# Optimization experiments

Measured on AMD Instinct MI355X. Metric: run time of the kernel, lower is better.

The kernel has to match this reference:

```python
import jax, jax.numpy as jnp
import numpy as np
from jax import lax

NL, DM, DI, DS, DTR, NC = 4, 128, 256, 16, 8, 256  # layers, d_model, d_inner, d_state, dt_rank, classes
B, L = 24, 3072  # conv stride 3 -> T = 1024


def _ln(x, w, b, eps=1e-5):
    mu = x.mean(-1, keepdims=True)
    v = ((x - mu) ** 2).mean(-1, keepdims=True)
    return (x - mu) * lax.rsqrt(v + eps) * w + b


def _mixer(h, inp, cw, cb, xp, dtw, dtb, Alog, D):
    # h: (B,T,DM) -> Mamba selective-scan mixer output (B,T,DI) before out_proj
    xz = h @ inp.T                                   # (B,T,2*DI)
    x, z = jnp.split(xz, 2, axis=-1)
    # causal depthwise conv (torch pads d_conv-1=3 both sides then slices [:T] == left-pad 3)
    xc = lax.conv_general_dilated(x.transpose(0, 2, 1), cw, (1,), [(3, 0)],
                                  feature_group_count=DI,
                                  dimension_numbers=('NCH', 'OIH', 'NCH'))
    xc = jax.nn.silu((xc + cb[None, :, None]).transpose(0, 2, 1))   # (B,T,DI)
    dbl = xc @ xp.T                                  # (B,T,DTR+2*DS)
    dt = jax.nn.softplus(dbl[..., :DTR] @ dtw.T + dtb)              # (B,T,DI)
    Bm, Cm = dbl[..., DTR:DTR + DS], dbl[..., DTR + DS:]            # (B,T,DS) each
    A = -jnp.exp(Alog)                               # (DI,DS)

    def step(hst, ins):
        dt_t, B_t, C_t, x_t = ins                    # (B,DI),(B,DS),(B,DS),(B,DI)
        hst = jnp.exp(dt_t[..., None] * A) * hst + (dt_t * x_t)[..., None] * B_t[:, None, :]
        return hst, jnp.einsum('bds,bs->bd', hst, C_t)

    h0 = jnp.zeros((h.shape[0], DI, DS), h.dtype)
    xs = (dt.transpose(1, 0, 2), Bm.transpose(1, 0, 2), Cm.transpose(1, 0, 2), xc.transpose(1, 0, 2))
    _, ys = lax.scan(step, h0, xs)                   # ys: (T,B,DI)
    y = ys.transpose(1, 0, 2) + D * xc
    return y * jax.nn.silu(z)


def _stack(h, p, nf_w, nf_b):
    residual = None
    for i in range(NL):
        residual = h if residual is None else h + residual
        hn = _ln(residual, p['lnw'][i], p['lnb'][i])
        y = _mixer(hn, p['inp'][i], p['cw'][i], p['cb'][i], p['xp'][i],
                   p['dtw'][i], p['dtb'][i], p['Alog'][i], p['D'][i])
        h = y @ p['outp'][i].T
    return _ln(h + residual, nf_w, nf_b)


def _forward(x, conv_w, conv_b, fp, bp, nf_w, nf_b, head_w, head_b):
    c = lax.conv_general_dilated(x[:, None, :], conv_w, (3,), [(1, 1)],
                                 dimension_numbers=('NCH', 'OIH', 'NCH'))
    h = (c + conv_b[None, :, None]).transpose(0, 2, 1)   # (B,T,DM)
    fw = _stack(h, fp, nf_w, nf_b)
    bw = _stack(h[:, ::-1, :], bp, nf_w, nf_b)
    comb = jnp.concatenate([fw[:, -1, :], bw[:, -1, :]], axis=-1)  # (B,2*DM)
    return comb @ head_w.T + head_b


def setup_inputs():
    key = jax.random.key(0)
    ks = iter(jax.random.split(key, 64))

    def rn(shape, s):
        return jax.random.normal(next(ks), shape, jnp.float32) * s

    def layer(prefix):
        dt0 = jnp.clip(jax.random.uniform(next(ks), (NL, DI)) * 0.1, 1e-3, None)
        return {
            prefix + '_inp': rn((NL, 2 * DI, DM), 0.05),
            prefix + '_cw': rn((NL, DI, 1, 4), 0.3),
            prefix + '_cb': rn((NL, DI), 0.02),
            prefix + '_xp': rn((NL, DTR + 2 * DS, DI), 0.05),
            prefix + '_dtw': rn((NL, DI, DTR), 0.1),
            prefix + '_dtb': jnp.log(jnp.expm1(dt0)),  # inverse-softplus of small positive dt
            prefix + '_Alog': jnp.log(jnp.broadcast_to(jnp.arange(1, DS + 1, dtype=jnp.float32), (NL, DI, DS))),
            prefix + '_D': jnp.ones((NL, DI), jnp.float32),
            prefix + '_outp': rn((NL, DM, DI), 0.05),
            prefix + '_lnw': jnp.ones((NL, DM), jnp.float32),
            prefix + '_lnb': jnp.zeros((NL, DM), jnp.float32),
        }

    inp = {'x': rn((B, L), 1.0), 'conv_w': rn((DM, 1, 3), 0.3), 'conv_b': jnp.zeros((DM,), jnp.float32)}
    inp.update(layer('f'))
    inp.update(layer('b'))
    inp.update({'nf_w': jnp.ones((DM,), jnp.float32), 'nf_b': jnp.zeros((DM,), jnp.float32),
                'head_w': rn((NC, 2 * DM), 0.05), 'head_b': jnp.zeros((NC,), jnp.float32)})
    return inp


def reference(x, conv_w, conv_b,
              f_inp, f_cw, f_cb, f_xp, f_dtw, f_dtb, f_Alog, f_D, f_outp, f_lnw, f_lnb,
              b_inp, b_cw, b_cb, b_xp, b_dtw, b_dtb, b_Alog, b_D, b_outp, b_lnw, b_lnb,
              nf_w, nf_b, head_w, head_b):
    fp = dict(inp=f_inp, cw=f_cw, cb=f_cb, xp=f_xp, dtw=f_dtw, dtb=f_dtb,
              Alog=f_Alog, D=f_D, outp=f_outp, lnw=f_lnw, lnb=f_lnb)
    bp = dict(inp=b_inp, cw=b_cw, cb=b_cb, xp=b_xp, dtw=b_dtw, dtb=b_dtb,
              Alog=b_Alog, D=b_D, outp=b_outp, lnw=b_lnw, lnb=b_lnb)
    return _forward(x, conv_w, conv_b, fp, bp, nf_w, nf_b, head_w, head_b)
```

## Files before the change

### kernel.cpp

```cpp
#include <hip/hip_runtime.h>
#include <hip/hip_bf16.h>
#include <math.h>

static constexpr int NL=4, DM=128, DI=256, DS=16, DTR=8, NC=256;
static constexpr int Bb=24, Lx=3072, T=1024;
static constexpr int ROWS = Bb*T;
static constexpr int NCH=8, TC=128;

typedef __attribute__((ext_vector_type(4))) float f32x4;
typedef __attribute__((ext_vector_type(8))) short bf16x8;

static __device__ inline unsigned short f2bf(float f){
  unsigned int u = __float_as_uint(f);
  unsigned int r = (u + 0x7FFFu + ((u >> 16) & 1u)) >> 16;
  return (unsigned short)r;
}

template<int CTRL>
static __device__ __forceinline__ float dpp_add(float x){
  int t = __builtin_amdgcn_update_dpp(0, __float_as_int(x), CTRL, 0xF, 0xF, true);
  return x + __int_as_float(t);
}
static __device__ __forceinline__ float row16_reduce(float x){
  x = dpp_add<0xB1>(x);
  x = dpp_add<0x4E>(x);
  x = dpp_add<0x114>(x);
  x = dpp_add<0x118>(x);
  return x;
}

__global__ __launch_bounds__(256) void k_conv0(const float* __restrict__ x,
    const float* __restrict__ cw, const float* __restrict__ cb,
    float* __restrict__ h0f, float* __restrict__ h0b){
  int idx = blockIdx.x*256 + threadIdx.x;
  int c = idx & (DM-1);
  int t = (idx >> 7) & (T-1);
  int b = idx >> 17;
  const float* xr = x + b*Lx;
  float acc = cb[c];
  int base = 3*t - 1;
#pragma unroll
  for (int k=0;k<3;k++){
    int j = base + k;
    float xv = (j>=0 && j<Lx) ? xr[j] : 0.f;
    acc = fmaf(xv, cw[c*3+k], acc);
  }
  h0f[(b*T + t)*DM + c] = acc;
  h0b[(b*T + (T-1-t))*DM + c] = acc;
}

__global__ __launch_bounds__(256) void k_cast(const float* __restrict__ src,
    unsigned short* __restrict__ dst, int n){
  int i = blockIdx.x*256 + threadIdx.x;
  if (i < n) dst[i] = f2bf(src[i]);
}

__global__ __launch_bounds__(256) void k_add_ln(const float* __restrict__ hin,
    float* __restrict__ res, const float* __restrict__ lnw, const float* __restrict__ lnb,
    unsigned short* __restrict__ hn, int first){
  int row = blockIdx.x*4 + (threadIdx.x >> 6);
  int lane = threadIdx.x & 63;
  const float* hr = hin + (long)row*DM;
  float* rr = res + (long)row*DM;
  float v0 = hr[lane], v1 = hr[lane+64];
  if (!first){ v0 += rr[lane]; v1 += rr[lane+64]; }
  rr[lane] = v0; rr[lane+64] = v1;
  float s = v0+v1;
#pragma unroll
  for (int m=1;m<64;m<<=1) s += __shfl_xor(s, m);
  float mu = s * (1.f/128.f);
  float d0 = v0-mu, d1 = v1-mu;
  float q = d0*d0 + d1*d1;
#pragma unroll
  for (int m=1;m<64;m<<=1) q += __shfl_xor(q, m);
  float rstd = rsqrtf(q*(1.f/128.f) + 1e-5f);
  hn[(long)row*DM+lane]    = f2bf(d0*rstd*lnw[lane]    + lnb[lane]);
  hn[(long)row*DM+lane+64] = f2bf(d1*rstd*lnw[lane+64] + lnb[lane+64]);
}

template<int N, int K>
__global__ __launch_bounds__(256) void k_mgemm(const unsigned short* __restrict__ A,
    const unsigned short* __restrict__ W, float* __restrict__ C){
  constexpr int BK = 32;
  __shared__ short As[128*BK];
  __shared__ short Ws[128*BK];
  int tid = threadIdx.x;
  int lane = tid & 63, wave = tid >> 6;
  int wr = (wave >> 1) * 64, wc = (wave & 1) * 64;
  long bm = blockIdx.x, bn = blockIdx.y;
  const short* Ag = (const short*)A + bm*128*K;
  const short* Wg = (const short*)W + bn*128*K;
  f32x4 acc[4][4] = {};
  int r = lane & 15, kg = (lane >> 4) * 8;
  for (int kb = 0; kb < K; kb += BK){
#pragma unroll
    for (int t = 0; t < 2; t++){
      int c = tid + t*256;
      int row = c >> 2, kc = (c & 3) * 8;
      *(bf16x8*)&As[row*BK + kc] = *(const bf16x8*)&Ag[row*K + kb + kc];
      *(bf16x8*)&Ws[row*BK + kc] = *(const bf16x8*)&Wg[row*K + kb + kc];
    }
    __syncthreads();
    bf16x8 af[4], wf[4];
#pragma unroll
    for (int m=0;m<4;m++) af[m] = *(const bf16x8*)&As[(wr + m*16 + r)*BK + kg];
#pragma unroll
    for (int n=0;n<4;n++) wf[n] = *(const bf16x8*)&Ws[(wc + n*16 + r)*BK + kg];
#pragma unroll
    for (int m=0;m<4;m++)
#pragma unroll
      for (int n=0;n<4;n++)
        acc[m][n] = __builtin_amdgcn_mfma_f32_16x16x32_bf16(af[m], wf[n], acc[m][n], 0, 0, 0);
    __syncthreads();
  }
  float* Cb = C + (bm*128)*N + bn*128;
  int rq = (lane >> 4) * 4, cn = lane & 15;
#pragma unroll
  for (int m=0;m<4;m++)
#pragma unroll
    for (int n=0;n<4;n++)
#pragma unroll
      for (int q=0;q<4;q++)
        Cb[(wr + m*16 + rq + q)*N + wc + n*16 + cn] = acc[m][n][q];
}

__global__ __launch_bounds__(256) void k_convs(const float* __restrict__ xz,
    const float* __restrict__ cw, const float* __restrict__ cb, float* __restrict__ xc){
  int idx = blockIdx.x*256 + threadIdx.x;
  int d = idx & (DI-1);
  int t = (idx >> 8) & (T-1);
  int b = idx >> 18;
  const float* xrow = xz + (long)b*T*2*DI;
  float acc = cb[d];
#pragma unroll
  for (int k=0;k<4;k++){
    int tt = t + k - 3;
    float xv = (tt>=0) ? xrow[(long)tt*2*DI + d] : 0.f;
    acc = fmaf(xv, cw[d*4+k], acc);
  }
  float s = acc / (1.f + __expf(-acc));
  xc[(long)(b*T+t)*DI + d] = s;
}

__global__ __launch_bounds__(256) void k_dbldt(const float* __restrict__ xc,
    const float* __restrict__ xp, const float* __restrict__ dtw, const float* __restrict__ dtb,
    float* __restrict__ gdt, float* __restrict__ bcg){
  __shared__ float xp_s[40][257];
  __shared__ float xc_s[16][257];
  __shared__ float dtw_s[DI][9];
  __shared__ float dtb_s[DI];
  __shared__ float dbl_s[16][41];
  int tid = threadIdx.x;
  long row0 = (long)blockIdx.x * 16;
  for (int lin = tid; lin < 40*DI; lin += 256){
    int n = lin >> 8, k = lin & 255;
    xp_s[n][k] = xp[lin];
  }
  for (int lin = tid; lin < DI*DTR; lin += 256)
    dtw_s[lin>>3][lin&7] = dtw[lin];
  dtb_s[tid] = dtb[tid];
  for (int lin = tid; lin < 16*DI; lin += 256){
    int r = lin >> 8, k = lin & 255;
    xc_s[r][k] = xc[(row0 + r)*DI + k];
  }
  __syncthreads();
  for (int idx = tid; idx < 16*40; idx += 256){
    int r = idx / 40, n = idx % 40;
    float acc = 0.f;
#pragma unroll 4
    for (int k=0;k<DI;k++) acc = fmaf(xc_s[r][k], xp_s[n][k], acc);
    dbl_s[r][n] = acc;
  }
  __syncthreads();
  {
    int d = tid;
    float w[8];
#pragma unroll
    for (int j=0;j<8;j++) w[j] = dtw_s[d][j];
    float bias = dtb_s[d];
    for (int r=0;r<16;r++){
      float acc = bias;
#pragma unroll
      for (int j=0;j<8;j++) acc = fmaf(dbl_s[r][j], w[j], acc);
      float sp = (acc > 20.f) ? acc : log1pf(__expf(acc));
      gdt[(row0 + r)*DI + d] = sp;
    }
  }
  for (int idx = tid; idx < 16*32; idx += 256){
    int r = idx >> 5, j = idx & 31;
    bcg[(row0 + r)*32 + j] = dbl_s[r][8 + j];
  }
}

__global__ __launch_bounds__(256) void k_scan1(const float* __restrict__ gdt,
    const float* __restrict__ bcg, const float* __restrict__ xc,
    const float* __restrict__ Alog, float* __restrict__ Pd, float* __restrict__ Hl){
  int b = blockIdx.z, ch = blockIdx.y, d0 = blockIdx.x*16;
  int tid = threadIdx.x, s = tid & 15, dl = tid >> 4, d = d0 + dl;
  float A = -__expf(Alog[d*DS + s]);
  __shared__ float dt_s[TC][16], x_s[TC][16], b_s[TC][16];
  long r0 = (long)b*T + ch*TC;
  for (int lin = tid; lin < TC*4; lin += 256){
    int i = lin >> 2, c4 = (lin & 3)*4;
    *(float4*)&dt_s[i][c4] = *(const float4*)&gdt[(r0+i)*DI + d0 + c4];
    *(float4*)&x_s[i][c4]  = *(const float4*)&xc [(r0+i)*DI + d0 + c4];
    *(float4*)&b_s[i][c4]  = *(const float4*)&bcg[(r0+i)*32 + c4];
  }
  __syncthreads();
  float h = 0.f, lp = 0.f;
  for (int i0 = 0; i0 < TC; i0 += 8){
    float dtv[8], xv[8], bv[8];
#pragma unroll
    for (int j=0;j<8;j++){ dtv[j]=dt_s[i0+j][dl]; xv[j]=x_s[i0+j][dl]; bv[j]=b_s[i0+j][s]; }
#pragma unroll
    for (int j=0;j<8;j++){
      float da = dtv[j]*A;
      lp += da;
      h = fmaf(__expf(da), h, dtv[j]*xv[j]*bv[j]);
    }
  }
  long o = ((long)(b*NCH + ch)*DI + d)*DS + s;
  Pd[o] = __expf(lp);
  Hl[o] = h;
}

__global__ __launch_bounds__(256) void k_scan2(const float* __restrict__ Pd,
    const float* __restrict__ Hl, float* __restrict__ Hst){
  int idx = blockIdx.x*256 + threadIdx.x;
  int b = idx >> 12, j = idx & 4095;
  long base = (long)b*NCH*4096 + j;
  float h = 0.f;
#pragma unroll
  for (int c=0;c<NCH;c++){
    Hst[base + c*4096] = h;
    h = Pd[base + c*4096]*h + Hl[base + c*4096];
  }
}

__global__ __launch_bounds__(256) void k_scan3(const float* __restrict__ gdt,
    const float* __restrict__ bcg, const float* __restrict__ xc, const float* __restrict__ xz,
    const float* __restrict__ Alog, const float* __restrict__ Dp,
    const float* __restrict__ Hst, unsigned short* __restrict__ yg){
  int b = blockIdx.z, ch = blockIdx.y, d0 = blockIdx.x*16;
  int tid = threadIdx.x, s = tid & 15, dl = tid >> 4, d = d0 + dl;
  float A = -__expf(Alog[d*DS + s]);
  float Dd = Dp[d];
  __shared__ float dt_s[TC][16], x_s[TC][16], z_s[TC][16], b_s[TC][16], c_s[TC][16];
  __shared__ float y_s[TC][16];
  long r0 = (long)b*T + ch*TC;
  for (int lin = tid; lin < TC*4; lin += 256){
    int i = lin >> 2, c4 = (lin & 3)*4;
    *(float4*)&dt_s[i][c4] = *(const float4*)&gdt[(r0+i)*DI + d0 + c4];
    *(float4*)&x_s[i][c4]  = *(const float4*)&xc [(r0+i)*DI + d0 + c4];
    float4 zv = *(const float4*)&xz [(r0+i)*2*DI + DI + d0 + c4];
    zv.x = zv.x/(1.f+__expf(-zv.x)); zv.y = zv.y/(1.f+__expf(-zv.y));
    zv.z = zv.z/(1.f+__expf(-zv.z)); zv.w = zv.w/(1.f+__expf(-zv.w));
    *(float4*)&z_s[i][c4]  = zv;
    *(float4*)&b_s[i][c4]  = *(const float4*)&bcg[(r0+i)*32 + c4];
    *(float4*)&c_s[i][c4]  = *(const float4*)&bcg[(r0+i)*32 + 16 + c4];
  }
  float h = Hst[((long)(b*NCH + ch)*DI + d)*DS + s];
  __syncthreads();
  for (int i0 = 0; i0 < TC; i0 += 8){
    float dtv[8], xv[8], bv[8], cv[8], dec[8], ad[8], p[8];
#pragma unroll
    for (int j=0;j<8;j++){
      dtv[j]=dt_s[i0+j][dl]; xv[j]=x_s[i0+j][dl];
      bv[j]=b_s[i0+j][s];    cv[j]=c_s[i0+j][s];
    }
#pragma unroll
    for (int j=0;j<8;j++){ dec[j] = __expf(dtv[j]*A); ad[j] = dtv[j]*xv[j]*bv[j]; }
#pragma unroll
    for (int j=0;j<8;j++){ h = fmaf(dec[j], h, ad[j]); p[j] = h * cv[j]; }
#pragma unroll
    for (int j=0;j<8;j++) p[j] = dpp_add<0xB1>(p[j]);
#pragma unroll
    for (int j=0;j<8;j++) p[j] = dpp_add<0x4E>(p[j]);
#pragma unroll
    for (int j=0;j<8;j++) p[j] = dpp_add<0x114>(p[j]);
#pragma unroll
    for (int j=0;j<8;j++) p[j] = dpp_add<0x118>(p[j]);
    if (s == 0){
#pragma unroll
      for (int j=0;j<8;j++)
        y_s[i0+j][dl] = fmaf(Dd, xv[j], p[j]) * z_s[i0+j][dl];
    }
  }
  __syncthreads();
  for (int lin = tid; lin < TC*2; lin += 256){
    int i = lin >> 1, dd8 = (lin & 1)*8;
    bf16x8 v;
#pragma unroll
    for (int k=0;k<8;k++) v[k] = (short)f2bf(y_s[i][dd8+k]);
    *(bf16x8*)&yg[(r0+i)*DI + d0 + dd8] = v;
  }
}

__global__ __launch_bounds__(64) void k_final(const float* __restrict__ hcur,
    const float* __restrict__ res, const float* __restrict__ nfw, const float* __restrict__ nfb,
    float* __restrict__ comb, int half){
  int b = blockIdx.x;
  int lane = threadIdx.x;
  const float* h = hcur + ((long)b*T + (T-1))*DM;
  const float* r = res  + ((long)b*T + (T-1))*DM;
  float v0 = h[lane]+r[lane], v1 = h[lane+64]+r[lane+64];
  float s = v0+v1;
#pragma unroll
  for (int m=1;m<64;m<<=1) s += __shfl_xor(s, m);
  float mu = s * (1.f/128.f);
  float d0 = v0-mu, d1 = v1-mu;
  float q = d0*d0 + d1*d1;
#pragma unroll
  for (int m=1;m<64;m<<=1) q += __shfl_xor(q, m);
  float rstd = rsqrtf(q*(1.f/128.f) + 1e-5f);
  comb[b*2*DM + half*DM + lane]    = d0*rstd*nfw[lane]    + nfb[lane];
  comb[b*2*DM + half*DM + lane+64] = d1*rstd*nfw[lane+64] + nfb[lane+64];
}

__global__ __launch_bounds__(256) void k_head(const float* __restrict__ comb,
    const float* __restrict__ hw, const float* __restrict__ hb, float* __restrict__ out){
  int b = blockIdx.x, n = threadIdx.x;
  const float* cr = comb + b*2*DM;
  float acc = hb[n];
#pragma unroll 4
  for (int k=0;k<2*DM;k++) acc = fmaf(cr[k], hw[n*2*DM + k], acc);
  out[b*NC + n] = acc;
}

extern "C" void kernel_launch(void* const* d_in, const int* in_sizes, int n_in,
                              void* d_out, int out_size, void* d_ws, size_t ws_size,
                              hipStream_t stream){
  auto F = [&](int i){ return (const float*)d_in[i]; };
  float* ws = (float*)d_ws;
  size_t o = 0;
  float* h0f = ws + o; o += (size_t)ROWS*DM;
  float* h0b = ws + o; o += (size_t)ROWS*DM;
  float* res = ws + o; o += (size_t)ROWS*DM;
  float* hcur= ws + o; o += (size_t)ROWS*DM;
  float* xz  = ws + o; o += (size_t)ROWS*2*DI;
  float* xc  = ws + o; o += (size_t)ROWS*DI;
  float* gdt = ws + o; o += (size_t)ROWS*DI;
  float* bcg = ws + o; o += (size_t)ROWS*2*DS;
  unsigned short* ybf = (unsigned short*)(ws + o); o += (size_t)ROWS*DI/2;
  unsigned short* hnbf = ybf;
  float* Pd  = ws + o; o += (size_t)Bb*NCH*DI*DS;
  float* Hl  = ws + o; o += (size_t)Bb*NCH*DI*DS;
  float* Hst = ws + o; o += (size_t)Bb*NCH*DI*DS;
  unsigned short* wbf = (unsigned short*)(ws + o); o += (size_t)2*NL*(2*DI*DM + DM*DI)/2;
  float* comb= ws + o; o += (size_t)Bb*2*DM;

  const int NI = NL*2*DI*DM;
  const int NO = NL*DM*DI;
  k_cast<<<(NI+255)/256, 256, 0, stream>>>(F(3),  wbf,            NI);
  k_cast<<<(NO+255)/256, 256, 0, stream>>>(F(11), wbf+NI,         NO);
  k_cast<<<(NI+255)/256, 256, 0, stream>>>(F(14), wbf+NI+NO,      NI);
  k_cast<<<(NO+255)/256, 256, 0, stream>>>(F(22), wbf+2*NI+NO,    NO);

  k_conv0<<<ROWS*DM/256, 256, 0, stream>>>(F(0), F(1), F(2), h0f, h0b);

  for (int dir = 0; dir < 2; dir++){
    int p = dir ? 14 : 3;
    const float* hin = dir ? h0b : h0f;
    unsigned short* winp  = wbf + (size_t)dir*(NI+NO);
    unsigned short* woutp = winp + NI;
    for (int l = 0; l < NL; l++){
      const float* hsrc = (l==0) ? hin : hcur;
      k_add_ln<<<ROWS/4, 256, 0, stream>>>(hsrc, res,
          F(p+9)+(size_t)l*DM, F(p+10)+(size_t)l*DM, hnbf, (l==0)?1:0);
      k_mgemm<2*DI, DM><<<dim3(ROWS/128, (2*DI)/128), 256, 0, stream>>>(
          hnbf, winp + (size_t)l*2*DI*DM, xz);
      k_convs<<<ROWS*DI/256, 256, 0, stream>>>(xz,
          F(p+1)+(size_t)l*DI*4, F(p+2)+(size_t)l*DI, xc);
      k_dbldt<<<ROWS/16, 256, 0, stream>>>(xc,
          F(p+3)+(size_t)l*(DTR+2*DS)*DI, F(p+4)+(size_t)l*DI*DTR,
          F(p+5)+(size_t)l*DI, gdt, bcg);
      k_scan1<<<dim3(DI/16, NCH, Bb), 256, 0, stream>>>(gdt, bcg, xc,
          F(p+6)+(size_t)l*DI*DS, Pd, Hl);
      k_scan2<<<(Bb*DI*DS)/256, 256, 0, stream>>>(Pd, Hl, Hst);
      k_scan3<<<dim3(DI/16, NCH, Bb), 256, 0, stream>>>(gdt, bcg, xc, xz,
          F(p+6)+(size_t)l*DI*DS, F(p+7)+(size_t)l*DI, Hst, ybf);
      k_mgemm<DM, DI><<<dim3(ROWS/128, DM/128), 256, 0, stream>>>(
          ybf, woutp + (size_t)l*DM*DI, hcur);
    }
    k_final<<<Bb, 64, 0, stream>>>(hcur, res, F(25), F(26), comb, dir);
  }
  k_head<<<Bb, 256, 0, stream>>>(comb, F(27), F(28), (float*)d_out);
}
```

Before: 1.836 ms.

## Compute x_proj with bf16 MFMA over 64-row tiles in dbldt kernel

The depthwise conv kernel now also writes a bf16 copy of its activations, and the x_proj weights are pre-cast to bf16. The dbldt kernel uses MFMA 16x16x32 instructions over 64-row tiles instead of scalar fp32 dot products over 16-row tiles. This removes the scalar FMA loop and the repeated per-block staging of the fp32 weight matrix. In exchange it adds an extra bf16 write per element and lowers the precision of dt, B and C, which feed the scan.

```diff
diff --git a/kernel.cpp b/kernel.cpp
--- a/kernel.cpp
+++ b/kernel.cpp
@@ -20,13 +20,6 @@
 static __device__ __forceinline__ float dpp_add(float x){
   int t = __builtin_amdgcn_update_dpp(0, __float_as_int(x), CTRL, 0xF, 0xF, true);
   return x + __int_as_float(t);
-}
-static __device__ __forceinline__ float row16_reduce(float x){
-  x = dpp_add<0xB1>(x);
-  x = dpp_add<0x4E>(x);
-  x = dpp_add<0x114>(x);
-  x = dpp_add<0x118>(x);
-  return x;
 }
 
 __global__ __launch_bounds__(256) void k_conv0(const float* __restrict__ x,
@@ -125,7 +118,8 @@
 }
 
 __global__ __launch_bounds__(256) void k_convs(const float* __restrict__ xz,
-    const float* __restrict__ cw, const float* __restrict__ cb, float* __restrict__ xc){
+    const float* __restrict__ cw, const float* __restrict__ cb,
+    float* __restrict__ xc, unsigned short* __restrict__ xcb){
   int idx = blockIdx.x*256 + threadIdx.x;
   int d = idx & (DI-1);
   int t = (idx >> 8) & (T-1);
@@ -139,56 +133,69 @@
     acc = fmaf(xv, cw[d*4+k], acc);
   }
   float s = acc / (1.f + __expf(-acc));
-  xc[(long)(b*T+t)*DI + d] = s;
-}
-
-__global__ __launch_bounds__(256) void k_dbldt(const float* __restrict__ xc,
-    const float* __restrict__ xp, const float* __restrict__ dtw, const float* __restrict__ dtb,
-    float* __restrict__ gdt, float* __restrict__ bcg){
-  __shared__ float xp_s[40][257];
-  __shared__ float xc_s[16][257];
-  __shared__ float dtw_s[DI][9];
-  __shared__ float dtb_s[DI];
-  __shared__ float dbl_s[16][41];
+  long o = (long)(b*T+t)*DI + d;
+  xc[o] = s;
+  xcb[o] = f2bf(s);
+}
+
+__global__ __launch_bounds__(256) void k_dbldt(const unsigned short* __restrict__ xcb,
+    const unsigned short* __restrict__ xpb, const float* __restrict__ dtw,
+    const float* __restrict__ dtb, float* __restrict__ gdt, float* __restrict__ bcg){
+  constexpr int BP = 264;
+  __shared__ short B_s[48*BP];
+  __shared__ float dbl_s[64][9];
+  __shared__ float bc_s[64][33];
   int tid = threadIdx.x;
-  long row0 = (long)blockIdx.x * 16;
-  for (int lin = tid; lin < 40*DI; lin += 256){
-    int n = lin >> 8, k = lin & 255;
-    xp_s[n][k] = xp[lin];
-  }
-  for (int lin = tid; lin < DI*DTR; lin += 256)
-    dtw_s[lin>>3][lin&7] = dtw[lin];
-  dtb_s[tid] = dtb[tid];
-  for (int lin = tid; lin < 16*DI; lin += 256){
-    int r = lin >> 8, k = lin & 255;
-    xc_s[r][k] = xc[(row0 + r)*DI + k];
+  int lane = tid & 63, wave = tid >> 6;
+  int wr = wave * 16;
+  long row0 = (long)blockIdx.x * 64;
+  float w[8];
+#pragma unroll
+  for (int j=0;j<8;j++) w[j] = dtw[tid*8 + j];
+  float bias = dtb[tid];
+  for (int c = tid; c < 48*32; c += 256){
+    int rowp = c >> 5, k8 = (c & 31) * 8;
+    bf16x8 v = {};
+    if (rowp < 40) v = *(const bf16x8*)&xpb[rowp*256 + k8];
+    *(bf16x8*)&B_s[rowp*BP + k8] = v;
   }
   __syncthreads();
-  for (int idx = tid; idx < 16*40; idx += 256){
-    int r = idx / 40, n = idx % 40;
-    float acc = 0.f;
-#pragma unroll 4
-    for (int k=0;k<DI;k++) acc = fmaf(xc_s[r][k], xp_s[n][k], acc);
-    dbl_s[r][n] = acc;
+  int cf = lane & 15, hi = lane >> 4;
+  const short* Ag = (const short*)xcb + (row0 + wr + cf)*DI + hi*8;
+  f32x4 acc[3] = {};
+#pragma unroll
+  for (int ks = 0; ks < 8; ks++){
+    bf16x8 af = *(const bf16x8*)&Ag[ks*32];
+#pragma unroll
+    for (int n = 0; n < 3; n++){
+      bf16x8 bf = *(const bf16x8*)&B_s[(n*16 + cf)*BP + ks*32 + hi*8];
+      acc[n] = __builtin_amdgcn_mfma_f32_16x16x32_bf16(af, bf, acc[n], 0, 0, 0);
+    }
+  }
+#pragma unroll
+  for (int n = 0; n < 3; n++){
+    int col = n*16 + cf;
+#pragma unroll
+    for (int q = 0; q < 4; q++){
+      int row = wr + hi*4 + q;
+      float v = acc[n][q];
+      if (col < 8)       dbl_s[row][col]    = v;
+      else if (col < 40) bc_s[row][col - 8] = v;
+    }
   }
   __syncthreads();
-  {
-    int d = tid;
-    float w[8];
-#pragma unroll
-    for (int j=0;j<8;j++) w[j] = dtw_s[d][j];
-    float bias = dtb_s[d];
-    for (int r=0;r<16;r++){
-      float acc = bias;
-#pragma unroll
-      for (int j=0;j<8;j++) acc = fmaf(dbl_s[r][j], w[j], acc);
-      float sp = (acc > 20.f) ? acc : log1pf(__expf(acc));
-      gdt[(row0 + r)*DI + d] = sp;
-    }
-  }
-  for (int idx = tid; idx < 16*32; idx += 256){
-    int r = idx >> 5, j = idx & 31;
-    bcg[(row0 + r)*32 + j] = dbl_s[r][8 + j];
+#pragma unroll
+  for (int i = 0; i < 8; i++){
+    int idx = tid + i*256;
+    int row = idx >> 5, col = idx & 31;
+    bcg[(row0 + row)*32 + col] = bc_s[row][col];
+  }
+  for (int r = 0; r < 64; r++){
+    float a = bias;
+#pragma unroll
+    for (int j = 0; j < 8; j++) a = fmaf(dbl_s[r][j], w[j], a);
+    float sp = (a > 20.f) ? a : log1pf(__expf(a));
+    gdt[(row0 + r)*DI + tid] = sp;
   }
 }
 
@@ -343,18 +350,23 @@
   float* bcg = ws + o; o += (size_t)ROWS*2*DS;
   unsigned short* ybf = (unsigned short*)(ws + o); o += (size_t)ROWS*DI/2;
   unsigned short* hnbf = ybf;
+  unsigned short* xcb  = ybf;
   float* Pd  = ws + o; o += (size_t)Bb*NCH*DI*DS;
   float* Hl  = ws + o; o += (size_t)Bb*NCH*DI*DS;
   float* Hst = ws + o; o += (size_t)Bb*NCH*DI*DS;
   unsigned short* wbf = (unsigned short*)(ws + o); o += (size_t)2*NL*(2*DI*DM + DM*DI)/2;
+  unsigned short* xpb = (unsigned short*)(ws + o); o += (size_t)2*NL*40*DI/2;
   float* comb= ws + o; o += (size_t)Bb*2*DM;
 
   const int NI = NL*2*DI*DM;
   const int NO = NL*DM*DI;
+  const int NX = NL*40*DI;
   k_cast<<<(NI+255)/256, 256, 0, stream>>>(F(3),  wbf,            NI);
   k_cast<<<(NO+255)/256, 256, 0, stream>>>(F(11), wbf+NI,         NO);
   k_cast<<<(NI+255)/256, 256, 0, stream>>>(F(14), wbf+NI+NO,      NI);
   k_cast<<<(NO+255)/256, 256, 0, stream>>>(F(22), wbf+2*NI+NO,    NO);
+  k_cast<<<(NX+255)/256, 256, 0, stream>>>(F(6),  xpb,            NX);
+  k_cast<<<(NX+255)/256, 256, 0, stream>>>(F(17), xpb+NX,         NX);
 
   k_conv0<<<ROWS*DM/256, 256, 0, stream>>>(F(0), F(1), F(2), h0f, h0b);
 
@@ -370,10 +382,10 @@
       k_mgemm<2*DI, DM><<<dim3(ROWS/128, (2*DI)/128), 256, 0, stream>>>(
           hnbf, winp + (size_t)l*2*DI*DM, xz);
       k_convs<<<ROWS*DI/256, 256, 0, stream>>>(xz,
-          F(p+1)+(size_t)l*DI*4, F(p+2)+(size_t)l*DI, xc);
-      k_dbldt<<<ROWS/16, 256, 0, stream>>>(xc,
-          F(p+3)+(size_t)l*(DTR+2*DS)*DI, F(p+4)+(size_t)l*DI*DTR,
-          F(p+5)+(size_t)l*DI, gdt, bcg);
+          F(p+1)+(size_t)l*DI*4, F(p+2)+(size_t)l*DI, xc, xcb);
+      k_dbldt<<<ROWS/64, 256, 0, stream>>>(xcb,
+          xpb + (size_t)(dir*NL + l)*40*DI,
+          F(p+4)+(size_t)l*DI*DTR, F(p+5)+(size_t)l*DI, gdt, bcg);
       k_scan1<<<dim3(DI/16, NCH, Bb), 256, 0, stream>>>(gdt, bcg, xc,
           F(p+6)+(size_t)l*DI*DS, Pd, Hl);
       k_scan2<<<(Bb*DI*DS)/256, 256, 0, stream>>>(Pd, Hl, Hst);
```

New measurement: 1.578 ms. 1.16x faster.
